# Kernel tuning notes

Hardware: AMD Instinct MI355X
Metric: run time of the kernel (lower is better)

## Reference

```python
import jax, jax.numpy as jnp
import numpy as np

N_NODES = 100000
N_EDGES = 1600000
N_FEAT = 500
N_CLASSES = 40


def gcn_conv(x, W, b, src, dst, n):
    """PyG GCNConv: add self-loops, symmetric deg normalization, linear + bias."""
    h = x @ W                                   # [n, out]
    loop = jnp.arange(n, dtype=src.dtype)
    s = jnp.concatenate([src, loop])            # sources incl. self-loops
    d = jnp.concatenate([dst, loop])            # destinations incl. self-loops
    deg = jax.ops.segment_sum(jnp.ones_like(d, dtype=x.dtype), d, num_segments=n)
    dinv = jax.lax.rsqrt(deg)                   # deg >= 1 because of self-loops
    norm = dinv[s] * dinv[d]                    # [E+n]
    out = jax.ops.segment_sum(h[s] * norm[:, None], d, num_segments=n)
    return out + b


def glorot(key, fan_in, fan_out):
    lim = np.sqrt(6.0 / (fan_in + fan_out)).astype(np.float32)
    return jax.random.uniform(key, (fan_in, fan_out), jnp.float32, -lim, lim)


def setup_inputs() -> dict:
    key = jax.random.key(0)
    ks = jax.random.split(key, 6)
    x = jax.random.normal(ks[0], (N_NODES, N_FEAT), dtype=jnp.float32)
    edge_index = jax.random.randint(ks[1], (2, N_EDGES), 0, N_NODES, dtype=jnp.int64)
    return {
        "x": x,
        "edge_index": edge_index,
        "W1": glorot(ks[2], N_FEAT, 128), "b1": jnp.zeros((128,), jnp.float32),
        "W2": glorot(ks[3], 128, 64),     "b2": jnp.zeros((64,), jnp.float32),
        "W4": glorot(ks[4], 64, N_CLASSES), "b4": jnp.zeros((N_CLASSES,), jnp.float32),
    }


def reference(x, edge_index, W1, b1, W2, b2, W4, b4):
    src, dst = edge_index[0], edge_index[1]
    n = x.shape[0]
    h = jax.nn.relu(gcn_conv(x, W1, b1, src, dst, n))
    h = jax.nn.relu(gcn_conv(h, W2, b2, src, dst, n))
    h = gcn_conv(h, W4, b4, src, dst, n)
    return jax.nn.log_softmax(h, axis=1)
```

## Files before the change

kernel.cpp:

```cpp
#include <hip/hip_runtime.h>
#include <hip/hip_bf16.h>
#include <cmath>

#define NNODES 100000
#define NEDGES 1600000
#define SCAN_B 1024

typedef __attribute__((ext_vector_type(8))) short bf16x8;
typedef __attribute__((ext_vector_type(4))) float f32x4;

__device__ __forceinline__ unsigned short f2bf(float f) {
    unsigned u = __builtin_bit_cast(unsigned, f);
    unsigned r = (u + 0x7fffu + ((u >> 16) & 1u)) >> 16;
    return (unsigned short)r;
}
__device__ __forceinline__ float bflo(unsigned v) {
    return __builtin_bit_cast(float, v << 16);
}
__device__ __forceinline__ float bfhi(unsigned v) {
    return __builtin_bit_cast(float, v & 0xffff0000u);
}


__global__ void zero_deg(int* __restrict__ deg, int n) {
    int i = blockIdx.x * 256 + threadIdx.x;
    if (i < n) deg[i] = 0;
}

__global__ __launch_bounds__(256) void count_deg_xcd(const int* __restrict__ dst,
                                                     int* __restrict__ deg, int E) {
    int g = blockIdx.x & 7;
    int sub = blockIdx.x >> 3;
    int nsub = gridDim.x >> 3;
    int lo = g * (NNODES / 8), hi = lo + (NNODES / 8);
    for (int e = sub * 256 + threadIdx.x; e < E; e += nsub * 256) {
        int d = dst[e];
        if (d >= lo && d < hi) atomicAdd(&deg[d], 1);
    }
}

__global__ void calc_dinv(const int* __restrict__ deg, float* __restrict__ dinv, int n) {
    int i = blockIdx.x * 256 + threadIdx.x;
    if (i < n) dinv[i] = rsqrtf(1.0f + (float)deg[i]);
}

__global__ __launch_bounds__(SCAN_B) void scan_block(const int* __restrict__ deg,
                                                     int* __restrict__ pos,
                                                     int* __restrict__ bsums, int n) {
    __shared__ int s[SCAN_B];
    int tid = threadIdx.x;
    int gid = blockIdx.x * SCAN_B + tid;
    int v = (gid < n) ? deg[gid] : 0;
    s[tid] = v;
    __syncthreads();
    for (int off = 1; off < SCAN_B; off <<= 1) {
        int t = (tid >= off) ? s[tid - off] : 0;
        __syncthreads();
        s[tid] += t;
        __syncthreads();
    }
    if (gid < n) pos[gid] = s[tid] - v;
    if (tid == SCAN_B - 1) bsums[blockIdx.x] = s[tid];
}

__global__ __launch_bounds__(128) void scan_sums(int* __restrict__ bsums, int nb) {
    __shared__ int s[128];
    int tid = threadIdx.x;
    int v = (tid < nb) ? bsums[tid] : 0;
    s[tid] = v;
    __syncthreads();
    for (int off = 1; off < 128; off <<= 1) {
        int t = (tid >= off) ? s[tid - off] : 0;
        __syncthreads();
        s[tid] += t;
        __syncthreads();
    }
    if (tid < nb) bsums[tid] = s[tid] - v;
}

__global__ __launch_bounds__(SCAN_B) void add_off(int* __restrict__ pos,
                                                  const int* __restrict__ bsums, int n) {
    int gid = blockIdx.x * SCAN_B + threadIdx.x;
    if (gid < n) pos[gid] += bsums[blockIdx.x];
}

__global__ __launch_bounds__(256) void csr_fill_xcd(const int* __restrict__ src,
                                                    const int* __restrict__ dst,
                                                    int* __restrict__ pos,
                                                    int* __restrict__ csr_src, int E) {
    int g = blockIdx.x & 7;
    int sub = blockIdx.x >> 3;
    int nsub = gridDim.x >> 3;
    int lo = g * (NNODES / 8), hi = lo + (NNODES / 8);
    for (int e = sub * 256 + threadIdx.x; e < E; e += nsub * 256) {
        int d = dst[e];
        if (d >= lo && d < hi) {
            int slot = atomicAdd(&pos[d], 1);
            csr_src[slot] = src[e];
        }
    }
}


__global__ __launch_bounds__(256) void conv_w1f(const float* __restrict__ W1,
                                                unsigned short* __restrict__ W1f) {
    int idx = blockIdx.x * 256 + threadIdx.x;
    if (idx >= 8192) return;
    int t = idx >> 9;
    int rest = idx & 511;
    int j = rest >> 6;
    int l = rest & 63;
    int n = j * 16 + (l & 15);
    int kb = t * 32 + (l >> 4) * 8;
    bf16x8 o;
    #pragma unroll
    for (int jj = 0; jj < 8; jj++) {
        int k = kb + jj;
        o[jj] = (k < 500) ? (short)f2bf(W1[k * 128 + n]) : (short)0;
    }
    *(bf16x8*)(W1f + (size_t)idx * 8) = o;
}

__global__ __launch_bounds__(256) void conv_w2f(const float* __restrict__ W2,
                                                unsigned short* __restrict__ W2f) {
    int idx = blockIdx.x * 256 + threadIdx.x;
    if (idx >= 1024) return;
    int t = idx >> 8;
    int rest = idx & 255;
    int j = rest >> 6;
    int l = rest & 63;
    int n = j * 16 + (l & 15);
    int kb = t * 32 + (l >> 4) * 8;
    bf16x8 o;
    #pragma unroll
    for (int jj = 0; jj < 8; jj++)
        o[jj] = (short)f2bf(W2[(kb + jj) * 64 + n]);
    *(bf16x8*)(W2f + (size_t)idx * 8) = o;
}

__device__ __forceinline__ bf16x8 load_a_frag(const float* __restrict__ abase, int k0, int q) {
    bf16x8 o;
    if (k0 + q * 8 + 8 <= 500) {
        float4 u = *(const float4*)(abase + k0);
        float4 v = *(const float4*)(abase + k0 + 4);
        o[0] = f2bf(u.x); o[1] = f2bf(u.y); o[2] = f2bf(u.z); o[3] = f2bf(u.w);
        o[4] = f2bf(v.x); o[5] = f2bf(v.y); o[6] = f2bf(v.z); o[7] = f2bf(v.w);
    } else {
        #pragma unroll
        for (int jj = 0; jj < 8; jj++) {
            int k = k0 + q * 8 + jj;
            o[jj] = (k < 500) ? (short)f2bf(abase[k0 + jj]) : (short)0;
        }
    }
    return o;
}


__global__ __launch_bounds__(256) void gemm1_mfma(
    const float* __restrict__ x, const unsigned short* __restrict__ W1f,
    const float* __restrict__ dinv, unsigned short* __restrict__ C, int M)
{
    const int tid = threadIdx.x;
    const int w = tid >> 6;
    const int l = tid & 63;
    const int lm = l & 15;
    const int q = l >> 4;
    const int row0 = blockIdx.x * 64;

    int r = row0 + w * 16 + lm;
    if (r >= M) r = M - 1;
    const float* abase = x + (size_t)r * 500 + q * 8;
    const unsigned short* bbase = W1f + (size_t)l * 8;

    f32x4 acc[8];
    #pragma unroll
    for (int j = 0; j < 8; j++) acc[j] = (f32x4){0.f, 0.f, 0.f, 0.f};

    bf16x8 a0, a1, b0[8], b1[8];

    a0 = load_a_frag(abase, 0, q);
    #pragma unroll
    for (int j = 0; j < 8; j++)
        b0[j] = *(const bf16x8*)(bbase + (size_t)j * 512);

    for (int tt = 0; tt < 8; ++tt) {
        const int t0 = 2 * tt, t1 = 2 * tt + 1;
        a1 = load_a_frag(abase, t1 * 32, q);
        #pragma unroll
        for (int j = 0; j < 8; j++)
            b1[j] = *(const bf16x8*)(bbase + (size_t)(t1 * 8 + j) * 512);
        #pragma unroll
        for (int j = 0; j < 8; j++)
            acc[j] = __builtin_amdgcn_mfma_f32_16x16x32_bf16(a0, b0[j], acc[j], 0, 0, 0);
        if (t0 + 2 < 16) {
            a0 = load_a_frag(abase, (t0 + 2) * 32, q);
            #pragma unroll
            for (int j = 0; j < 8; j++)
                b0[j] = *(const bf16x8*)(bbase + (size_t)((t0 + 2) * 8 + j) * 512);
        }
        #pragma unroll
        for (int j = 0; j < 8; j++)
            acc[j] = __builtin_amdgcn_mfma_f32_16x16x32_bf16(a1, b1[j], acc[j], 0, 0, 0);
    }

    #pragma unroll
    for (int reg = 0; reg < 4; reg++) {
        int grow = row0 + w * 16 + q * 4 + reg;
        if (grow < M) {
            float d = dinv[grow];
            #pragma unroll
            for (int j = 0; j < 8; j++)
                C[(size_t)grow * 128 + j * 16 + lm] = f2bf(d * acc[j][reg]);
        }
    }
}


__global__ __launch_bounds__(256) void gemm2_mfma(
    const unsigned short* __restrict__ A, const unsigned short* __restrict__ W2f,
    const float* __restrict__ dinv, unsigned short* __restrict__ C, int M)
{
    const int tid = threadIdx.x;
    const int w = tid >> 6;
    const int l = tid & 63;
    const int lm = l & 15;
    const int q = l >> 4;
    const int row0 = blockIdx.x * 128;

    const unsigned short* abase[2];
    #pragma unroll
    for (int i = 0; i < 2; i++) {
        int r = row0 + w * 32 + i * 16 + lm;
        if (r >= M) r = M - 1;
        abase[i] = A + (size_t)r * 128 + q * 8;
    }

    f32x4 acc[2][4];
    #pragma unroll
    for (int i = 0; i < 2; i++)
        #pragma unroll
        for (int j = 0; j < 4; j++) acc[i][j] = (f32x4){0.f, 0.f, 0.f, 0.f};

    for (int t = 0; t < 4; ++t) {
        const int k0 = t * 32;
        bf16x8 af[2];
        #pragma unroll
        for (int i = 0; i < 2; i++)
            af[i] = *(const bf16x8*)(abase[i] + k0);
        bf16x8 bfr[4];
        #pragma unroll
        for (int j = 0; j < 4; j++)
            bfr[j] = *(const bf16x8*)(W2f + (((size_t)t * 4 + j) * 64 + l) * 8);
        #pragma unroll
        for (int i = 0; i < 2; i++)
            #pragma unroll
            for (int j = 0; j < 4; j++)
                acc[i][j] = __builtin_amdgcn_mfma_f32_16x16x32_bf16(af[i], bfr[j], acc[i][j], 0, 0, 0);
    }

    #pragma unroll
    for (int i = 0; i < 2; i++) {
        #pragma unroll
        for (int reg = 0; reg < 4; reg++) {
            int grow = row0 + w * 32 + i * 16 + q * 4 + reg;
            if (grow < M) {
                float d = dinv[grow];
                #pragma unroll
                for (int j = 0; j < 4; j++)
                    C[(size_t)grow * 64 + j * 16 + lm] = f2bf(d * acc[i][j][reg]);
            }
        }
    }
}


__global__ __launch_bounds__(256) void gemm_n40(
    const float* __restrict__ A, const float* __restrict__ W,
    const float* __restrict__ bias, const float* __restrict__ dinv,
    float* __restrict__ C, int M)
{
    __shared__ float sA[32][65];
    __shared__ float sW[64][40];
    const int row0 = blockIdx.x * 32;
    for (int idx = threadIdx.x; idx < 64 * 40; idx += 256)
        sW[idx / 40][idx % 40] = W[idx];
    for (int idx = threadIdx.x; idx < 32 * 64; idx += 256) {
        int r = idx >> 6, k = idx & 63;
        int row = row0 + r;
        float v = 0.0f;
        if (row < M) v = fmaxf(A[(long)row * 64 + k] + bias[k], 0.0f);
        sA[r][k] = v;
    }
    __syncthreads();
    float acc[5] = {0, 0, 0, 0, 0};
    int rr[5], cc[5];
    #pragma unroll
    for (int j = 0; j < 5; j++) {
        int o = threadIdx.x + 256 * j;
        rr[j] = o / 40; cc[j] = o % 40;
    }
    for (int k = 0; k < 64; k++) {
        #pragma unroll
        for (int j = 0; j < 5; j++) acc[j] += sA[rr[j]][k] * sW[k][cc[j]];
    }
    #pragma unroll
    for (int j = 0; j < 5; j++) {
        int row = row0 + rr[j];
        if (row < M) C[(long)row * 40 + cc[j]] = dinv[row] * acc[j];
    }
}


template<int F, bool OBF16>
__global__ __launch_bounds__(256) void gather_bf(
    const unsigned short* __restrict__ h, const float* __restrict__ dinv,
    const int* __restrict__ pos, const int* __restrict__ csr_src,
    void* __restrict__ outv, const float* __restrict__ bias, int n)
{
    constexpr int P = F / 2;
    unsigned t = blockIdx.x * 256u + threadIdx.x;
    unsigned node = t / P;
    unsigned p = t - node * P;
    if (node >= (unsigned)n) return;
    int e0 = node ? pos[node - 1] : 0;
    int e1 = pos[node];
    float di = dinv[node];
    unsigned sv = *(const unsigned*)(h + (size_t)node * F + 2 * p);
    float a0 = bflo(sv);
    float a1 = bfhi(sv);
    int j = e0;
    for (; j + 4 <= e1; j += 4) {
        int s0 = csr_src[j], s1 = csr_src[j + 1], s2 = csr_src[j + 2], s3 = csr_src[j + 3];
        unsigned v0 = *(const unsigned*)(h + (size_t)s0 * F + 2 * p);
        unsigned v1 = *(const unsigned*)(h + (size_t)s1 * F + 2 * p);
        unsigned v2 = *(const unsigned*)(h + (size_t)s2 * F + 2 * p);
        unsigned v3 = *(const unsigned*)(h + (size_t)s3 * F + 2 * p);
        a0 += bflo(v0) + bflo(v1) + bflo(v2) + bflo(v3);
        a1 += bfhi(v0) + bfhi(v1) + bfhi(v2) + bfhi(v3);
    }
    for (; j < e1; j++) {
        int s = csr_src[j];
        unsigned v = *(const unsigned*)(h + (size_t)s * F + 2 * p);
        a0 += bflo(v);
        a1 += bfhi(v);
    }
    a0 *= di; a1 *= di;
    if constexpr (OBF16) {
        a0 = fmaxf(a0 + bias[2 * p], 0.0f);
        a1 = fmaxf(a1 + bias[2 * p + 1], 0.0f);
        ((unsigned*)outv)[(size_t)node * P + p] =
            ((unsigned)f2bf(a1) << 16) | (unsigned)f2bf(a0);
    } else {
        float2 r; r.x = a0; r.y = a1;
        ((float2*)outv)[(size_t)node * P + p] = r;
    }
}


template<int F>
__global__ __launch_bounds__(256) void gather_agg(
    const float* __restrict__ h, const float* __restrict__ dinv,
    const int* __restrict__ pos, const int* __restrict__ csr_src,
    float* __restrict__ out, int n)
{
    unsigned t = blockIdx.x * 256u + threadIdx.x;
    unsigned node = t / F;
    unsigned c = t - node * F;
    if (node >= (unsigned)n) return;
    int e0 = node ? pos[node - 1] : 0;
    int e1 = pos[node];
    float di = dinv[node];
    float acc = h[(size_t)node * F + c];
    int j = e0;
    for (; j + 4 <= e1; j += 4) {
        int s0 = csr_src[j], s1 = csr_src[j + 1], s2 = csr_src[j + 2], s3 = csr_src[j + 3];
        float v0 = h[(size_t)s0 * F + c];
        float v1 = h[(size_t)s1 * F + c];
        float v2 = h[(size_t)s2 * F + c];
        float v3 = h[(size_t)s3 * F + c];
        acc += v0 + v1 + v2 + v3;
    }
    for (; j < e1; j++) {
        int s = csr_src[j];
        acc += h[(size_t)s * F + c];
    }
    out[(size_t)node * F + c] = di * acc;
}


__global__ __launch_bounds__(256) void logsoftmax40(const float* __restrict__ h,
                                                    const float* __restrict__ bias,
                                                    float* __restrict__ out, int n) {
    int wave = (blockIdx.x * 256 + threadIdx.x) >> 6;
    int lane = threadIdx.x & 63;
    if (wave >= n) return;
    float x = 0.0f, v = -INFINITY;
    if (lane < 40) { x = h[(long)wave * 40 + lane] + bias[lane]; v = x; }
    #pragma unroll
    for (int off = 32; off; off >>= 1) v = fmaxf(v, __shfl_xor(v, off, 64));
    float ex = (lane < 40) ? expf(x - v) : 0.0f;
    float s = ex;
    #pragma unroll
    for (int off = 32; off; off >>= 1) s += __shfl_xor(s, off, 64);
    if (lane < 40) out[(long)wave * 40 + lane] = x - v - logf(s);
}


extern "C" void kernel_launch(void* const* d_in, const int* in_sizes, int n_in,
                              void* d_out, int out_size, void* d_ws, size_t ws_size,
                              hipStream_t stream) {
    const float* x  = (const float*)d_in[0];
    const int*   ei = (const int*)d_in[1];
    const float* W1 = (const float*)d_in[2];
    const float* b1 = (const float*)d_in[3];
    const float* W2 = (const float*)d_in[4];
    const float* b2 = (const float*)d_in[5];
    const float* W4 = (const float*)d_in[6];
    const float* b4 = (const float*)d_in[7];
    float* out = (float*)d_out;
    float* ws  = (float*)d_ws;

    const int N = NNODES, E = NEDGES;
    const int* src = ei;
    const int* dst = ei + E;

    float*          dinv    = ws;
    int*            deg     = (int*)(ws + 100000);
    int*            pos     = (int*)(ws + 200000);
    int*            bsums   = (int*)(ws + 300000);
    int*            csr_src = (int*)(ws + 300200);
    unsigned short* W1f     = (unsigned short*)(ws + 1900200);
    unsigned short* W2f     = (unsigned short*)(ws + 1933000);
    unsigned short* h1      = (unsigned short*)(ws + 1937100);
    unsigned short* h2      = (unsigned short*)(ws + 1937100);
    unsigned short* a1      = (unsigned short*)(ws + 8337100);
    float*          h3      = ws + 8337100;
    float*          a2      = ws + 14737100;
    float*          a3      = out;

    const int nscan = (N + SCAN_B - 1) / SCAN_B;

    zero_deg<<<(N + 255) / 256, 256, 0, stream>>>(deg, N);
    count_deg_xcd<<<1024, 256, 0, stream>>>(dst, deg, E);
    calc_dinv<<<(N + 255) / 256, 256, 0, stream>>>(deg, dinv, N);
    scan_block<<<nscan, SCAN_B, 0, stream>>>(deg, pos, bsums, N);
    scan_sums<<<1, 128, 0, stream>>>(bsums, nscan);
    add_off<<<nscan, SCAN_B, 0, stream>>>(pos, bsums, N);
    csr_fill_xcd<<<1024, 256, 0, stream>>>(src, dst, pos, csr_src, E);

    conv_w1f<<<32, 256, 0, stream>>>(W1, W1f);
    conv_w2f<<<4, 256, 0, stream>>>(W2, W2f);

    gemm1_mfma<<<(N + 63) / 64, 256, 0, stream>>>(x, W1f, dinv, h1, N);
    {
        unsigned tot = (unsigned)N * 64u;
        gather_bf<128, true><<<(tot + 255) / 256, 256, 0, stream>>>(h1, dinv, pos, csr_src, a1, b1, N);
    }

    gemm2_mfma<<<(N + 127) / 128, 256, 0, stream>>>(a1, W2f, dinv, h2, N);
    {
        unsigned tot = (unsigned)N * 32u;
        gather_bf<64, false><<<(tot + 255) / 256, 256, 0, stream>>>(h2, dinv, pos, csr_src, a2, nullptr, N);
    }

    gemm_n40<<<(N + 31) / 32, 256, 0, stream>>>(a2, W4, b2, dinv, h3, N);
    {
        unsigned tot = (unsigned)N * 40u;
        gather_agg<40><<<(tot + 255) / 256, 256, 0, stream>>>(h3, dinv, pos, csr_src, a3, N);
    }

    logsoftmax40<<<(N * 64 + 255) / 256, 256, 0, stream>>>(a3, b4, out, N);
}
```

Measured before the change: 765.4 us.

## Stage gemm1 A and B tiles through LDS with async global_load_lds double buffering

Rewrites the first GEMM's main loop so the fp32 x tiles and the pre-swizzled W1 fragments are copied straight into double-buffered shared memory with global_load_lds. Only one wave loads B per block, where before every wave loaded it. The last partial K tile is handled in registers. This targets redundant B traffic and register-held prefetch, but adds a block barrier and vmcnt wait every K step, which may serialize loads and compute.

```diff
diff --git a/kernel.cpp b/kernel.cpp
--- a/kernel.cpp
+++ b/kernel.cpp
@@ -19,6 +19,12 @@
 }
 __device__ __forceinline__ float bfhi(unsigned v) {
     return __builtin_bit_cast(float, v & 0xffff0000u);
+}
+
+__device__ __forceinline__ void gload16(const void* g, void* l) {
+    __builtin_amdgcn_global_load_lds(
+        (const __attribute__((address_space(1))) unsigned int*)g,
+        (__attribute__((address_space(3))) unsigned int*)l, 16, 0, 0);
 }
 
 
@@ -138,70 +144,79 @@
     *(bf16x8*)(W2f + (size_t)idx * 8) = o;
 }
 
-__device__ __forceinline__ bf16x8 load_a_frag(const float* __restrict__ abase, int k0, int q) {
-    bf16x8 o;
-    if (k0 + q * 8 + 8 <= 500) {
-        float4 u = *(const float4*)(abase + k0);
-        float4 v = *(const float4*)(abase + k0 + 4);
-        o[0] = f2bf(u.x); o[1] = f2bf(u.y); o[2] = f2bf(u.z); o[3] = f2bf(u.w);
-        o[4] = f2bf(v.x); o[5] = f2bf(v.y); o[6] = f2bf(v.z); o[7] = f2bf(v.w);
-    } else {
-        #pragma unroll
-        for (int jj = 0; jj < 8; jj++) {
-            int k = k0 + q * 8 + jj;
-            o[jj] = (k < 500) ? (short)f2bf(abase[k0 + jj]) : (short)0;
-        }
-    }
-    return o;
-}
-
 
 __global__ __launch_bounds__(256) void gemm1_mfma(
     const float* __restrict__ x, const unsigned short* __restrict__ W1f,
     const float* __restrict__ dinv, unsigned short* __restrict__ C, int M)
 {
+    __shared__ float sA[2][2048];
+    __shared__ unsigned short sB[2][4096];
     const int tid = threadIdx.x;
     const int w = tid >> 6;
     const int l = tid & 63;
     const int lm = l & 15;
     const int q = l >> 4;
+    const int l4 = l * 4;
     const int row0 = blockIdx.x * 64;
 
     int r = row0 + w * 16 + lm;
     if (r >= M) r = M - 1;
     const float* abase = x + (size_t)r * 500 + q * 8;
-    const unsigned short* bbase = W1f + (size_t)l * 8;
 
     f32x4 acc[8];
     #pragma unroll
     for (int j = 0; j < 8; j++) acc[j] = (f32x4){0.f, 0.f, 0.f, 0.f};
 
-    bf16x8 a0, a1, b0[8], b1[8];
-
-    a0 = load_a_frag(abase, 0, q);
-    #pragma unroll
-    for (int j = 0; j < 8; j++)
-        b0[j] = *(const bf16x8*)(bbase + (size_t)j * 512);
-
-    for (int tt = 0; tt < 8; ++tt) {
-        const int t0 = 2 * tt, t1 = 2 * tt + 1;
-        a1 = load_a_frag(abase, t1 * 32, q);
-        #pragma unroll
-        for (int j = 0; j < 8; j++)
-            b1[j] = *(const bf16x8*)(bbase + (size_t)(t1 * 8 + j) * 512);
-        #pragma unroll
-        for (int j = 0; j < 8; j++)
-            acc[j] = __builtin_amdgcn_mfma_f32_16x16x32_bf16(a0, b0[j], acc[j], 0, 0, 0);
-        if (t0 + 2 < 16) {
-            a0 = load_a_frag(abase, (t0 + 2) * 32, q);
+    auto STAGE = [&](int buf, int t) {
+        const float* g0 = abase + t * 32;
+        gload16(g0,     &sA[buf][w * 512 + 0]);
+        gload16(g0 + 4, &sA[buf][w * 512 + 256]);
+        if (w == 0) {
             #pragma unroll
             for (int j = 0; j < 8; j++)
-                b0[j] = *(const bf16x8*)(bbase + (size_t)((t0 + 2) * 8 + j) * 512);
-        }
-        #pragma unroll
-        for (int j = 0; j < 8; j++)
-            acc[j] = __builtin_amdgcn_mfma_f32_16x16x32_bf16(a1, b1[j], acc[j], 0, 0, 0);
-    }
+                gload16(W1f + (((size_t)t * 8 + j) * 64 + l) * 8, &sB[buf][j * 512]);
+        }
+    };
+
+    STAGE(0, 0);
+    asm volatile("s_waitcnt vmcnt(0)" ::: "memory");
+    __syncthreads();
+
+    bf16x8 a15;
+    bf16x8 b15[8];
+    int buf = 0;
+    for (int t = 0; t < 15; ++t) {
+        if (t < 14) {
+            STAGE(buf ^ 1, t + 1);
+        } else {
+            bf16x8 o;
+            #pragma unroll
+            for (int jj = 0; jj < 8; jj++) {
+                int k = 480 + q * 8 + jj;
+                o[jj] = (k < 500) ? (short)f2bf(abase[480 + jj]) : (short)0;
+            }
+            a15 = o;
+            #pragma unroll
+            for (int j = 0; j < 8; j++)
+                b15[j] = *(const bf16x8*)(W1f + (((size_t)15 * 8 + j) * 64 + l) * 8);
+        }
+        float4 u = *(const float4*)&sA[buf][w * 512 + l4];
+        float4 v = *(const float4*)&sA[buf][w * 512 + 256 + l4];
+        bf16x8 af;
+        af[0] = f2bf(u.x); af[1] = f2bf(u.y); af[2] = f2bf(u.z); af[3] = f2bf(u.w);
+        af[4] = f2bf(v.x); af[5] = f2bf(v.y); af[6] = f2bf(v.z); af[7] = f2bf(v.w);
+        #pragma unroll
+        for (int j = 0; j < 8; j++) {
+            bf16x8 bfr = *(const bf16x8*)&sB[buf][j * 512 + l * 8];
+            acc[j] = __builtin_amdgcn_mfma_f32_16x16x32_bf16(af, bfr, acc[j], 0, 0, 0);
+        }
+        asm volatile("s_waitcnt vmcnt(0)" ::: "memory");
+        __syncthreads();
+        buf ^= 1;
+    }
+    #pragma unroll
+    for (int j = 0; j < 8; j++)
+        acc[j] = __builtin_amdgcn_mfma_f32_16x16x32_bf16(a15, b15[j], acc[j], 0, 0, 0);
 
     #pragma unroll
     for (int reg = 0; reg < 4; reg++) {
```

Result: no change. 757.4 us (-1.0%).
